# Kernel tuning notes

Hardware: AMD Instinct MI355X
Metric: run time of the kernel (lower is better)

The kernel has to match this reference:

```python
import jax, jax.numpy as jnp
import numpy as np

NUM_GRAPHS = 4096  # fixed number of segments for scatter_mean


def setup_inputs() -> dict:
    key = jax.random.key(0)
    ks = jax.random.split(key, 8)
    N, D, G = 1_000_000, 256, 256
    s = 1.0 / np.sqrt(D)
    x = jax.random.normal(ks[0], (N, D), dtype=jnp.float32)
    batch = jnp.sort(jax.random.randint(ks[1], (N,), 0, NUM_GRAPHS, dtype=jnp.int64))
    W = jax.random.normal(ks[2], (D, G), dtype=jnp.float32) * s
    b = jax.random.normal(ks[3], (G,), dtype=jnp.float32) * s
    Wg = jax.random.normal(ks[4], (D, G), dtype=jnp.float32) * s
    bg = jax.random.normal(ks[5], (G,), dtype=jnp.float32) * s
    Wf = jax.random.normal(ks[6], (G, G), dtype=jnp.float32) * (1.0 / np.sqrt(G))
    bf = jax.random.normal(ks[7], (G,), dtype=jnp.float32) * (1.0 / np.sqrt(G))
    return {"x": x, "batch": batch, "W": W, "b": b, "Wg": Wg, "bg": bg, "Wf": Wf, "bf": bf}


def reference(x, batch, W, b, Wg, bg, Wf, bf):
    # gated linear: states * softmax(gates) over feature dim (dim=1)
    states = x @ W + b                                   # [N, G]
    gates = jax.nn.softmax(x @ Wg + bg, axis=1)          # [N, G]
    gated = states * gates                               # [N, G]
    # scatter_mean over graph ids
    seg_sum = jax.ops.segment_sum(gated, batch, num_segments=NUM_GRAPHS)
    counts = jax.ops.segment_sum(jnp.ones((x.shape[0],), dtype=gated.dtype), batch,
                                 num_segments=NUM_GRAPHS)
    mean = seg_sum / jnp.maximum(counts, 1.0)[:, None]   # [NUM_GRAPHS, G]
    return mean @ Wf + bf
```

## Files before the change

kernel.cpp:

```cpp
#include <hip/hip_runtime.h>
#include <hip/hip_bf16.h>

typedef __attribute__((ext_vector_type(8))) short short8;
typedef __attribute__((ext_vector_type(4))) float f32x4;

#define D_DIM 256
#define G_DIM 256
#define NSEG 4096
#define BM 64

__device__ __forceinline__ unsigned f2bf_u(float f) {
  unsigned u = __builtin_bit_cast(unsigned, f);
  return (u + 0x7fffu + ((u >> 16) & 1u)) >> 16;
}
__device__ __forceinline__ unsigned pk_bf2(float a, float b) {
  __hip_bfloat162 h = __float22bfloat162_rn(float2{a, b});
  unsigned r;
  __builtin_memcpy(&r, &h, 4);
  return r;
}

template <int CTRL>
__device__ __forceinline__ float dpp_add(float v) {
  int x = __builtin_bit_cast(int, v);
  int y = __builtin_amdgcn_update_dpp(0, x, CTRL, 0xF, 0xF, true);
  return v + __builtin_bit_cast(float, y);
}
__device__ __forceinline__ float row16_sum(float v) {
  v = dpp_add<0xB1>(v);
  v = dpp_add<0x4E>(v);
  v = dpp_add<0x124>(v);
  v = dpp_add<0x128>(v);
  return v;
}

__global__ void wconv_kernel(const float* __restrict__ W, const float* __restrict__ Wg,
                             unsigned short* __restrict__ Wc) {
  int j = blockIdx.x;
  int k = threadIdx.x;
  float v = (j < 256) ? W[k * 256 + j] : Wg[k * 256 + (j - 256)];
  Wc[j * 256 + k] = (unsigned short)f2bf_u(v);
}

__global__ void count_kernel(const int* __restrict__ batch, int N, float* __restrict__ counts) {
  int g = blockIdx.x * blockDim.x + threadIdx.x;
  if (g >= NSEG) return;
  int lo = 0, hi = N;
  while (lo < hi) { int mid = (lo + hi) >> 1; if (batch[mid] < g) lo = mid + 1; else hi = mid; }
  int lo2 = lo, hi2 = N;
  while (lo2 < hi2) { int mid = (lo2 + hi2) >> 1; if (batch[mid] < g + 1) lo2 = mid + 1; else hi2 = mid; }
  counts[g] = (float)(lo2 - lo);
}

__global__ __launch_bounds__(512, 4) void fused_main(
    const float* __restrict__ x, const int* __restrict__ batch,
    const unsigned short* __restrict__ Wc,
    const float* __restrict__ bvec, const float* __restrict__ bgvec,
    float* __restrict__ seg, int N) {
  __shared__ __align__(16) char xs[32768];
  __shared__ __align__(16) float part[8][64];
  __shared__ __align__(16) float sinv[64];

  const int t = threadIdx.x;
  const int lane = t & 63;
  const int wid = t >> 6;
  const int lr = lane & 15;
  const int lk = lane >> 4;
  const long row0 = (long)blockIdx.x * BM;

#pragma unroll
  for (int it = 0; it < 4; ++it) {
    int rl = it * 16 + (t >> 5);
    int kb = (t & 31) * 8;
    const float4* p = (const float4*)(x + (row0 + rl) * D_DIM + kb);
    float4 v0 = p[0], v1 = p[1];
    uint4 pk;
    pk.x = pk_bf2(v0.x, v0.y);
    pk.y = pk_bf2(v0.z, v0.w);
    pk.z = pk_bf2(v1.x, v1.y);
    pk.w = pk_bf2(v1.z, v1.w);
    int byte = (rl * 512 + kb * 2) ^ ((rl & 7) << 4);
    *(uint4*)(xs + byte) = pk;
  }
  __syncthreads();

  f32x4 acc[4][4];
#pragma unroll
  for (int m = 0; m < 4; ++m)
#pragma unroll
    for (int n = 0; n < 4; ++n) acc[m][n] = (f32x4){0.f, 0.f, 0.f, 0.f};

  const int cb = wid * 32;
  __builtin_amdgcn_s_setprio(1);
#pragma unroll
  for (int kk = 0; kk < 8; ++kk) {
    const int k0 = kk * 32 + lk * 8;
    short8 a[4], bb[4];
#pragma unroll
    for (int n = 0; n < 4; ++n) {
      int col = (n < 2) ? (cb + n * 16 + lr) : (256 + cb + (n - 2) * 16 + lr);
      bb[n] = *(const short8*)(Wc + col * 256 + k0);
    }
#pragma unroll
    for (int m = 0; m < 4; ++m) {
      int row = m * 16 + lr;
      int byte = (row * 512 + k0 * 2) ^ ((row & 7) << 4);
      a[m] = *(const short8*)(xs + byte);
    }
#pragma unroll
    for (int m = 0; m < 4; ++m)
#pragma unroll
      for (int n = 0; n < 4; ++n)
        acc[m][n] = __builtin_amdgcn_mfma_f32_16x16x32_bf16(a[m], bb[n], acc[m][n], 0, 0, 0);
  }
  __builtin_amdgcn_s_setprio(0);

  int rb[4][4];
#pragma unroll
  for (int m = 0; m < 4; ++m) {
    const int4 v = *(const int4*)(batch + row0 + m * 16 + lk * 4);
    rb[m][0] = v.x; rb[m][1] = v.y; rb[m][2] = v.z; rb[m][3] = v.w;
  }
  const int g0 = batch[row0];
  const int g1 = batch[row0 + BM - 1];

  float bgv[2];
#pragma unroll
  for (int n = 0; n < 2; ++n) bgv[n] = bgvec[cb + n * 16 + lr];
#pragma unroll
  for (int m = 0; m < 4; ++m)
#pragma unroll
    for (int n = 2; n < 4; ++n)
#pragma unroll
      for (int q = 0; q < 4; ++q)
        acc[m][n][q] = __expf(acc[m][n][q] + bgv[n - 2]);

#pragma unroll
  for (int m = 0; m < 4; ++m) {
    float s[4];
#pragma unroll
    for (int q = 0; q < 4; ++q) s[q] = row16_sum(acc[m][2][q] + acc[m][3][q]);
    if (lr == 0) {
#pragma unroll
      for (int q = 0; q < 4; ++q) part[wid][m * 16 + lk * 4 + q] = s[q];
    }
  }
  __syncthreads();
  if (wid == 0) {
    float v = part[0][lane] + part[1][lane] + part[2][lane] + part[3][lane] +
              part[4][lane] + part[5][lane] + part[6][lane] + part[7][lane];
    sinv[lane] = 1.0f / v;
  }
  __syncthreads();

  float bv[2];
#pragma unroll
  for (int n = 0; n < 2; ++n) bv[n] = bvec[cb + n * 16 + lr];
  f32x4 siv[4];
#pragma unroll
  for (int m = 0; m < 4; ++m) siv[m] = *(const f32x4*)(&sinv[m * 16 + lk * 4]);
#pragma unroll
  for (int m = 0; m < 4; ++m)
#pragma unroll
    for (int n = 0; n < 2; ++n)
#pragma unroll
      for (int q = 0; q < 4; ++q)
        acc[m][n][q] = (acc[m][n][q] + bv[n]) * acc[m][n + 2][q] * siv[m][q];

  for (int g = g0; g <= g1; ++g) {
    float p[2] = {0.f, 0.f};
#pragma unroll
    for (int m = 0; m < 4; ++m)
#pragma unroll
      for (int q = 0; q < 4; ++q) {
        bool hit = (rb[m][q] == g);
#pragma unroll
        for (int n = 0; n < 2; ++n) p[n] += hit ? acc[m][n][q] : 0.f;
      }
#pragma unroll
    for (int n = 0; n < 2; ++n) {
      p[n] += __shfl_xor(p[n], 16);
      p[n] += __shfl_xor(p[n], 32);
    }
    if (lane < 16) {
#pragma unroll
      for (int n = 0; n < 2; ++n)
        atomicAdd(seg + (long)g * G_DIM + cb + n * 16 + lane, p[n]);
    }
  }
}

__global__ __launch_bounds__(256) void final_kernel(
    float* __restrict__ seg, const float* __restrict__ counts,
    const float* __restrict__ Wf, const float* __restrict__ bfv) {
  __shared__ float mlds[16][257];
  int g0 = blockIdx.x * 16;
  int t = threadIdx.x;
#pragma unroll
  for (int i = 0; i < 16; ++i) {
    float inv = 1.0f / fmaxf(counts[g0 + i], 1.0f);
    mlds[i][t] = seg[(g0 + i) * 256 + t] * inv;
  }
  __syncthreads();
  float a[16];
#pragma unroll
  for (int i = 0; i < 16; ++i) a[i] = 0.f;
  for (int k = 0; k < 256; ++k) {
    float w = Wf[k * 256 + t];
#pragma unroll
    for (int i = 0; i < 16; ++i) a[i] += mlds[i][k] * w;
  }
  float bfx = bfv[t];
#pragma unroll
  for (int i = 0; i < 16; ++i) seg[(g0 + i) * 256 + t] = a[i] + bfx;
}

extern "C" void kernel_launch(void* const* d_in, const int* in_sizes, int n_in,
                              void* d_out, int out_size, void* d_ws, size_t ws_size,
                              hipStream_t stream) {
  const float* x = (const float*)d_in[0];
  const int* batch = (const int*)d_in[1];
  const float* W = (const float*)d_in[2];
  const float* b = (const float*)d_in[3];
  const float* Wg = (const float*)d_in[4];
  const float* bg = (const float*)d_in[5];
  const float* Wf = (const float*)d_in[6];
  const float* bf = (const float*)d_in[7];
  const int N = in_sizes[0] / D_DIM;

  unsigned short* Wc = (unsigned short*)d_ws;
  float* counts = (float*)((char*)d_ws + 262144);
  float* seg = (float*)d_out;

  (void)hipMemsetAsync(d_out, 0, (size_t)out_size * sizeof(float), stream);
  hipLaunchKernelGGL(wconv_kernel, dim3(512), dim3(256), 0, stream, W, Wg, Wc);
  hipLaunchKernelGGL(count_kernel, dim3(NSEG / 256), dim3(256), 0, stream, batch, N, counts);
  hipLaunchKernelGGL(fused_main, dim3(N / BM), dim3(512), 0, stream, x, batch, Wc, b, bg, seg, N);
  hipLaunchKernelGGL(final_kernel, dim3(NSEG / 16), dim3(256), 0, stream, seg, counts, Wf, bf);
}
```

Baseline: 638.9 us.

## Use persistent blocks over contiguous tile ranges and fold output zeroing into count kernel

```diff
diff --git a/kernel.cpp b/kernel.cpp
--- a/kernel.cpp
+++ b/kernel.cpp
@@ -8,6 +8,7 @@
 #define G_DIM 256
 #define NSEG 4096
 #define BM 64
+#define NBLK 2048
 
 __device__ __forceinline__ unsigned f2bf_u(float f) {
   unsigned u = __builtin_bit_cast(unsigned, f);
@@ -42,8 +43,13 @@
   Wc[j * 256 + k] = (unsigned short)f2bf_u(v);
 }
 
-__global__ void count_kernel(const int* __restrict__ batch, int N, float* __restrict__ counts) {
+__global__ void count_kernel(const int* __restrict__ batch, int N, float* __restrict__ counts,
+                             float* __restrict__ seg) {
   int g = blockIdx.x * blockDim.x + threadIdx.x;
+  float4* s4 = (float4*)seg;
+  const float4 z = {0.f, 0.f, 0.f, 0.f};
+#pragma unroll
+  for (int i = 0; i < (NSEG * G_DIM / 4) / (NSEG); ++i) s4[i * NSEG + g] = z;
   if (g >= NSEG) return;
   int lo = 0, hi = N;
   while (lo < hi) { int mid = (lo + hi) >> 1; if (batch[mid] < g) lo = mid + 1; else hi = mid; }
@@ -66,126 +72,136 @@
   const int wid = t >> 6;
   const int lr = lane & 15;
   const int lk = lane >> 4;
-  const long row0 = (long)blockIdx.x * BM;
-
-#pragma unroll
-  for (int it = 0; it < 4; ++it) {
-    int rl = it * 16 + (t >> 5);
-    int kb = (t & 31) * 8;
-    const float4* p = (const float4*)(x + (row0 + rl) * D_DIM + kb);
-    float4 v0 = p[0], v1 = p[1];
-    uint4 pk;
-    pk.x = pk_bf2(v0.x, v0.y);
-    pk.y = pk_bf2(v0.z, v0.w);
-    pk.z = pk_bf2(v1.x, v1.y);
-    pk.w = pk_bf2(v1.z, v1.w);
-    int byte = (rl * 512 + kb * 2) ^ ((rl & 7) << 4);
-    *(uint4*)(xs + byte) = pk;
-  }
-  __syncthreads();
-
-  f32x4 acc[4][4];
-#pragma unroll
-  for (int m = 0; m < 4; ++m)
-#pragma unroll
-    for (int n = 0; n < 4; ++n) acc[m][n] = (f32x4){0.f, 0.f, 0.f, 0.f};
-
   const int cb = wid * 32;
-  __builtin_amdgcn_s_setprio(1);
-#pragma unroll
-  for (int kk = 0; kk < 8; ++kk) {
-    const int k0 = kk * 32 + lk * 8;
-    short8 a[4], bb[4];
-#pragma unroll
-    for (int n = 0; n < 4; ++n) {
-      int col = (n < 2) ? (cb + n * 16 + lr) : (256 + cb + (n - 2) * 16 + lr);
-      bb[n] = *(const short8*)(Wc + col * 256 + k0);
-    }
+  const int ntiles = N / BM;
+
+  const int q = ntiles / NBLK, r = ntiles % NBLK;
+  const int bid = blockIdx.x;
+  const int c0 = bid * q + (bid < r ? bid : r);
+  const int c1 = c0 + q + (bid < r ? 1 : 0);
+
+  float bgv[2], bv[2];
+#pragma unroll
+  for (int n = 0; n < 2; ++n) {
+    bgv[n] = bgvec[cb + n * 16 + lr];
+    bv[n] = bvec[cb + n * 16 + lr];
+  }
+
+  for (int tile = c0; tile < c1; ++tile) {
+    const long row0 = (long)tile * BM;
+
+#pragma unroll
+    for (int it = 0; it < 4; ++it) {
+      int rl = it * 16 + (t >> 5);
+      int kb = (t & 31) * 8;
+      const float4* p = (const float4*)(x + (row0 + rl) * D_DIM + kb);
+      float4 v0 = p[0], v1 = p[1];
+      uint4 pk;
+      pk.x = pk_bf2(v0.x, v0.y);
+      pk.y = pk_bf2(v0.z, v0.w);
+      pk.z = pk_bf2(v1.x, v1.y);
+      pk.w = pk_bf2(v1.z, v1.w);
+      int byte = (rl * 512 + kb * 2) ^ ((rl & 7) << 4);
+      *(uint4*)(xs + byte) = pk;
+    }
+    __syncthreads();
+
+    f32x4 acc[4][4];
+#pragma unroll
+    for (int m = 0; m < 4; ++m)
+#pragma unroll
+      for (int n = 0; n < 4; ++n) acc[m][n] = (f32x4){0.f, 0.f, 0.f, 0.f};
+
+    __builtin_amdgcn_s_setprio(1);
+#pragma unroll
+    for (int kk = 0; kk < 8; ++kk) {
+      const int k0 = kk * 32 + lk * 8;
+      short8 a[4], bb[4];
+#pragma unroll
+      for (int n = 0; n < 4; ++n) {
+        int col = (n < 2) ? (cb + n * 16 + lr) : (256 + cb + (n - 2) * 16 + lr);
+        bb[n] = *(const short8*)(Wc + col * 256 + k0);
+      }
+#pragma unroll
+      for (int m = 0; m < 4; ++m) {
+        int row = m * 16 + lr;
+        int byte = (row * 512 + k0 * 2) ^ ((row & 7) << 4);
+        a[m] = *(const short8*)(xs + byte);
+      }
+#pragma unroll
+      for (int m = 0; m < 4; ++m)
+#pragma unroll
+        for (int n = 0; n < 4; ++n)
+          acc[m][n] = __builtin_amdgcn_mfma_f32_16x16x32_bf16(a[m], bb[n], acc[m][n], 0, 0, 0);
+    }
+    __builtin_amdgcn_s_setprio(0);
+
+    int rb[4][4];
 #pragma unroll
     for (int m = 0; m < 4; ++m) {
-      int row = m * 16 + lr;
-      int byte = (row * 512 + k0 * 2) ^ ((row & 7) << 4);
-      a[m] = *(const short8*)(xs + byte);
-    }
+      const int4 v = *(const int4*)(batch + row0 + m * 16 + lk * 4);
+      rb[m][0] = v.x; rb[m][1] = v.y; rb[m][2] = v.z; rb[m][3] = v.w;
+    }
+    const int g0 = batch[row0];
+    const int g1 = batch[row0 + BM - 1];
+
 #pragma unroll
     for (int m = 0; m < 4; ++m)
 #pragma unroll
-      for (int n = 0; n < 4; ++n)
-        acc[m][n] = __builtin_amdgcn_mfma_f32_16x16x32_bf16(a[m], bb[n], acc[m][n], 0, 0, 0);
-  }
-  __builtin_amdgcn_s_setprio(0);
-
-  int rb[4][4];
-#pragma unroll
-  for (int m = 0; m < 4; ++m) {
-    const int4 v = *(const int4*)(batch + row0 + m * 16 + lk * 4);
-    rb[m][0] = v.x; rb[m][1] = v.y; rb[m][2] = v.z; rb[m][3] = v.w;
-  }
-  const int g0 = batch[row0];
-  const int g1 = batch[row0 + BM - 1];
-
-  float bgv[2];
-#pragma unroll
-  for (int n = 0; n < 2; ++n) bgv[n] = bgvec[cb + n * 16 + lr];
-#pragma unroll
-  for (int m = 0; m < 4; ++m)
-#pragma unroll
-    for (int n = 2; n < 4; ++n)
-#pragma unroll
-      for (int q = 0; q < 4; ++q)
-        acc[m][n][q] = __expf(acc[m][n][q] + bgv[n - 2]);
-
-#pragma unroll
-  for (int m = 0; m < 4; ++m) {
-    float s[4];
-#pragma unroll
-    for (int q = 0; q < 4; ++q) s[q] = row16_sum(acc[m][2][q] + acc[m][3][q]);
-    if (lr == 0) {
-#pragma unroll
-      for (int q = 0; q < 4; ++q) part[wid][m * 16 + lk * 4 + q] = s[q];
-    }
-  }
-  __syncthreads();
-  if (wid == 0) {
-    float v = part[0][lane] + part[1][lane] + part[2][lane] + part[3][lane] +
-              part[4][lane] + part[5][lane] + part[6][lane] + part[7][lane];
-    sinv[lane] = 1.0f / v;
-  }
-  __syncthreads();
-
-  float bv[2];
-#pragma unroll
-  for (int n = 0; n < 2; ++n) bv[n] = bvec[cb + n * 16 + lr];
-  f32x4 siv[4];
-#pragma unroll
-  for (int m = 0; m < 4; ++m) siv[m] = *(const f32x4*)(&sinv[m * 16 + lk * 4]);
-#pragma unroll
-  for (int m = 0; m < 4; ++m)
-#pragma unroll
-    for (int n = 0; n < 2; ++n)
-#pragma unroll
-      for (int q = 0; q < 4; ++q)
-        acc[m][n][q] = (acc[m][n][q] + bv[n]) * acc[m][n + 2][q] * siv[m][q];
-
-  for (int g = g0; g <= g1; ++g) {
-    float p[2] = {0.f, 0.f};
+      for (int n = 2; n < 4; ++n)
+#pragma unroll
+        for (int qq = 0; qq < 4; ++qq)
+          acc[m][n][qq] = __expf(acc[m][n][qq] + bgv[n - 2]);
+
+#pragma unroll
+    for (int m = 0; m < 4; ++m) {
+      float s[4];
+#pragma unroll
+      for (int qq = 0; qq < 4; ++qq) s[qq] = row16_sum(acc[m][2][qq] + acc[m][3][qq]);
+      if (lr == 0) {
+#pragma unroll
+        for (int qq = 0; qq < 4; ++qq) part[wid][m * 16 + lk * 4 + qq] = s[qq];
+      }
+    }
+    __syncthreads();
+    if (wid == 0) {
+      float v = part[0][lane] + part[1][lane] + part[2][lane] + part[3][lane] +
+                part[4][lane] + part[5][lane] + part[6][lane] + part[7][lane];
+      sinv[lane] = 1.0f / v;
+    }
+    __syncthreads();
+
+    f32x4 siv[4];
+#pragma unroll
+    for (int m = 0; m < 4; ++m) siv[m] = *(const f32x4*)(&sinv[m * 16 + lk * 4]);
 #pragma unroll
     for (int m = 0; m < 4; ++m)
 #pragma unroll
-      for (int q = 0; q < 4; ++q) {
-        bool hit = (rb[m][q] == g);
-#pragma unroll
-        for (int n = 0; n < 2; ++n) p[n] += hit ? acc[m][n][q] : 0.f;
-      }
-#pragma unroll
-    for (int n = 0; n < 2; ++n) {
-      p[n] += __shfl_xor(p[n], 16);
-      p[n] += __shfl_xor(p[n], 32);
-    }
-    if (lane < 16) {
-#pragma unroll
       for (int n = 0; n < 2; ++n)
-        atomicAdd(seg + (long)g * G_DIM + cb + n * 16 + lane, p[n]);
+#pragma unroll
+        for (int qq = 0; qq < 4; ++qq)
+          acc[m][n][qq] = (acc[m][n][qq] + bv[n]) * acc[m][n + 2][qq] * siv[m][qq];
+
+    for (int g = g0; g <= g1; ++g) {
+      float p[2] = {0.f, 0.f};
+#pragma unroll
+      for (int m = 0; m < 4; ++m)
+#pragma unroll
+        for (int qq = 0; qq < 4; ++qq) {
+          bool hit = (rb[m][qq] == g);
+#pragma unroll
+          for (int n = 0; n < 2; ++n) p[n] += hit ? acc[m][n][qq] : 0.f;
+        }
+#pragma unroll
+      for (int n = 0; n < 2; ++n) {
+        p[n] += __shfl_xor(p[n], 16);
+        p[n] += __shfl_xor(p[n], 32);
+      }
+      if (lane < 16) {
+#pragma unroll
+        for (int n = 0; n < 2; ++n)
+          atomicAdd(seg + (long)g * G_DIM + cb + n * 16 + lane, p[n]);
+      }
     }
   }
 }
@@ -232,9 +248,8 @@
   float* counts = (float*)((char*)d_ws + 262144);
   float* seg = (float*)d_out;
 
-  (void)hipMemsetAsync(d_out, 0, (size_t)out_size * sizeof(float), stream);
   hipLaunchKernelGGL(wconv_kernel, dim3(512), dim3(256), 0, stream, W, Wg, Wc);
-  hipLaunchKernelGGL(count_kernel, dim3(NSEG / 256), dim3(256), 0, stream, batch, N, counts);
-  hipLaunchKernelGGL(fused_main, dim3(N / BM), dim3(512), 0, stream, x, batch, Wc, b, bg, seg, N);
+  hipLaunchKernelGGL(count_kernel, dim3(NSEG / 256), dim3(256), 0, stream, batch, N, counts, seg);
+  hipLaunchKernelGGL(fused_main, dim3(NBLK), dim3(512), 0, stream, x, batch, Wc, b, bg, seg, N);
   hipLaunchKernelGGL(final_kernel, dim3(NSEG / 16), dim3(256), 0, stream, seg, counts, Wf, bf);
 }
```

Measured after the change: 1.151 ms. +80.1%, slower.

## Split GEMM into gate then state passes to cut registers and raise occupancy

Applied to the files above, without the earlier changes.

```diff
diff --git a/kernel.cpp b/kernel.cpp
--- a/kernel.cpp
+++ b/kernel.cpp
@@ -18,6 +18,12 @@
   unsigned r;
   __builtin_memcpy(&r, &h, 4);
   return r;
+}
+__device__ __forceinline__ float unpk_lo(unsigned u) {
+  return __builtin_bit_cast(float, u << 16);
+}
+__device__ __forceinline__ float unpk_hi(unsigned u) {
+  return __builtin_bit_cast(float, u & 0xffff0000u);
 }
 
 template <int CTRL>
@@ -42,8 +48,13 @@
   Wc[j * 256 + k] = (unsigned short)f2bf_u(v);
 }
 
-__global__ void count_kernel(const int* __restrict__ batch, int N, float* __restrict__ counts) {
+__global__ void count_kernel(const int* __restrict__ batch, int N, float* __restrict__ counts,
+                             float* __restrict__ seg) {
   int g = blockIdx.x * blockDim.x + threadIdx.x;
+  float4* s4 = (float4*)seg;
+  const float4 z = {0.f, 0.f, 0.f, 0.f};
+#pragma unroll
+  for (int i = 0; i < 64; ++i) s4[i * NSEG + g] = z;
   if (g >= NSEG) return;
   int lo = 0, hi = N;
   while (lo < hi) { int mid = (lo + hi) >> 1; if (batch[mid] < g) lo = mid + 1; else hi = mid; }
@@ -52,7 +63,7 @@
   counts[g] = (float)(lo2 - lo);
 }
 
-__global__ __launch_bounds__(512, 4) void fused_main(
+__global__ __launch_bounds__(512, 6) void fused_main(
     const float* __restrict__ x, const int* __restrict__ batch,
     const unsigned short* __restrict__ Wc,
     const float* __restrict__ bvec, const float* __restrict__ bgvec,
@@ -67,6 +78,7 @@
   const int lr = lane & 15;
   const int lk = lane >> 4;
   const long row0 = (long)blockIdx.x * BM;
+  const int cb = wid * 32;
 
 #pragma unroll
   for (int it = 0; it < 4; ++it) {
@@ -84,62 +96,58 @@
   }
   __syncthreads();
 
-  f32x4 acc[4][4];
+  f32x4 acc[4][2];
+
 #pragma unroll
   for (int m = 0; m < 4; ++m)
 #pragma unroll
-    for (int n = 0; n < 4; ++n) acc[m][n] = (f32x4){0.f, 0.f, 0.f, 0.f};
-
-  const int cb = wid * 32;
+    for (int n = 0; n < 2; ++n) acc[m][n] = (f32x4){0.f, 0.f, 0.f, 0.f};
+
   __builtin_amdgcn_s_setprio(1);
 #pragma unroll
   for (int kk = 0; kk < 8; ++kk) {
     const int k0 = kk * 32 + lk * 8;
-    short8 a[4], bb[4];
-#pragma unroll
-    for (int n = 0; n < 4; ++n) {
-      int col = (n < 2) ? (cb + n * 16 + lr) : (256 + cb + (n - 2) * 16 + lr);
-      bb[n] = *(const short8*)(Wc + col * 256 + k0);
-    }
-#pragma unroll
-    for (int m = 0; m < 4; ++m) {
-      int row = m * 16 + lr;
-      int byte = (row * 512 + k0 * 2) ^ ((row & 7) << 4);
-      a[m] = *(const short8*)(xs + byte);
-    }
+    short8 bb[2];
+#pragma unroll
+    for (int n = 0; n < 2; ++n)
+      bb[n] = *(const short8*)(Wc + (256 + cb + n * 16 + lr) * 256 + k0);
+#pragma unroll
+    for (int mb = 0; mb < 2; ++mb) {
+      short8 a[2];
+#pragma unroll
+      for (int mi = 0; mi < 2; ++mi) {
+        int row = (mb * 2 + mi) * 16 + lr;
+        int byte = (row * 512 + k0 * 2) ^ ((row & 7) << 4);
+        a[mi] = *(const short8*)(xs + byte);
+      }
+#pragma unroll
+      for (int mi = 0; mi < 2; ++mi)
+#pragma unroll
+        for (int n = 0; n < 2; ++n)
+          acc[mb * 2 + mi][n] =
+              __builtin_amdgcn_mfma_f32_16x16x32_bf16(a[mi], bb[n], acc[mb * 2 + mi][n], 0, 0, 0);
+    }
+  }
+  __builtin_amdgcn_s_setprio(0);
+
+  {
+    float bgv[2];
+#pragma unroll
+    for (int n = 0; n < 2; ++n) bgv[n] = bgvec[cb + n * 16 + lr];
 #pragma unroll
     for (int m = 0; m < 4; ++m)
 #pragma unroll
-      for (int n = 0; n < 4; ++n)
-        acc[m][n] = __builtin_amdgcn_mfma_f32_16x16x32_bf16(a[m], bb[n], acc[m][n], 0, 0, 0);
-  }
-  __builtin_amdgcn_s_setprio(0);
-
-  int rb[4][4];
-#pragma unroll
-  for (int m = 0; m < 4; ++m) {
-    const int4 v = *(const int4*)(batch + row0 + m * 16 + lk * 4);
-    rb[m][0] = v.x; rb[m][1] = v.y; rb[m][2] = v.z; rb[m][3] = v.w;
-  }
-  const int g0 = batch[row0];
-  const int g1 = batch[row0 + BM - 1];
-
-  float bgv[2];
-#pragma unroll
-  for (int n = 0; n < 2; ++n) bgv[n] = bgvec[cb + n * 16 + lr];
-#pragma unroll
-  for (int m = 0; m < 4; ++m)
-#pragma unroll
-    for (int n = 2; n < 4; ++n)
-#pragma unroll
-      for (int q = 0; q < 4; ++q)
-        acc[m][n][q] = __expf(acc[m][n][q] + bgv[n - 2]);
+      for (int n = 0; n < 2; ++n)
+#pragma unroll
+        for (int q = 0; q < 4; ++q)
+          acc[m][n][q] = __expf(acc[m][n][q] + bgv[n]);
+  }
 
 #pragma unroll
   for (int m = 0; m < 4; ++m) {
     float s[4];
 #pragma unroll
-    for (int q = 0; q < 4; ++q) s[q] = row16_sum(acc[m][2][q] + acc[m][3][q]);
+    for (int q = 0; q < 4; ++q) s[q] = row16_sum(acc[m][0][q] + acc[m][1][q]);
     if (lr == 0) {
 #pragma unroll
       for (int q = 0; q < 4; ++q) part[wid][m * 16 + lk * 4 + q] = s[q];
@@ -153,19 +161,72 @@
   }
   __syncthreads();
 
-  float bv[2];
-#pragma unroll
-  for (int n = 0; n < 2; ++n) bv[n] = bvec[cb + n * 16 + lr];
-  f32x4 siv[4];
-#pragma unroll
-  for (int m = 0; m < 4; ++m) siv[m] = *(const f32x4*)(&sinv[m * 16 + lk * 4]);
+  unsigned pkk[4][2][2];
+#pragma unroll
+  for (int m = 0; m < 4; ++m) {
+    f32x4 siv = *(const f32x4*)(&sinv[m * 16 + lk * 4]);
+#pragma unroll
+    for (int n = 0; n < 2; ++n) {
+      pkk[m][n][0] = pk_bf2(acc[m][n][0] * siv[0], acc[m][n][1] * siv[1]);
+      pkk[m][n][1] = pk_bf2(acc[m][n][2] * siv[2], acc[m][n][3] * siv[3]);
+    }
+  }
+
 #pragma unroll
   for (int m = 0; m < 4; ++m)
 #pragma unroll
+    for (int n = 0; n < 2; ++n) acc[m][n] = (f32x4){0.f, 0.f, 0.f, 0.f};
+
+  __builtin_amdgcn_s_setprio(1);
+#pragma unroll
+  for (int kk = 0; kk < 8; ++kk) {
+    const int k0 = kk * 32 + lk * 8;
+    short8 bb[2];
+#pragma unroll
     for (int n = 0; n < 2; ++n)
-#pragma unroll
-      for (int q = 0; q < 4; ++q)
-        acc[m][n][q] = (acc[m][n][q] + bv[n]) * acc[m][n + 2][q] * siv[m][q];
+      bb[n] = *(const short8*)(Wc + (cb + n * 16 + lr) * 256 + k0);
+#pragma unroll
+    for (int mb = 0; mb < 2; ++mb) {
+      short8 a[2];
+#pragma unroll
+      for (int mi = 0; mi < 2; ++mi) {
+        int row = (mb * 2 + mi) * 16 + lr;
+        int byte = (row * 512 + k0 * 2) ^ ((row & 7) << 4);
+        a[mi] = *(const short8*)(xs + byte);
+      }
+#pragma unroll
+      for (int mi = 0; mi < 2; ++mi)
+#pragma unroll
+        for (int n = 0; n < 2; ++n)
+          acc[mb * 2 + mi][n] =
+              __builtin_amdgcn_mfma_f32_16x16x32_bf16(a[mi], bb[n], acc[mb * 2 + mi][n], 0, 0, 0);
+    }
+  }
+  __builtin_amdgcn_s_setprio(0);
+
+  int rb[4][4];
+#pragma unroll
+  for (int m = 0; m < 4; ++m) {
+    const int4 v = *(const int4*)(batch + row0 + m * 16 + lk * 4);
+    rb[m][0] = v.x; rb[m][1] = v.y; rb[m][2] = v.z; rb[m][3] = v.w;
+  }
+  const int g0 = batch[row0];
+  const int g1 = batch[row0 + BM - 1];
+
+  {
+    float bv[2];
+#pragma unroll
+    for (int n = 0; n < 2; ++n) bv[n] = bvec[cb + n * 16 + lr];
+#pragma unroll
+    for (int m = 0; m < 4; ++m)
+#pragma unroll
+      for (int n = 0; n < 2; ++n) {
+        acc[m][n][0] = (acc[m][n][0] + bv[n]) * unpk_lo(pkk[m][n][0]);
+        acc[m][n][1] = (acc[m][n][1] + bv[n]) * unpk_hi(pkk[m][n][0]);
+        acc[m][n][2] = (acc[m][n][2] + bv[n]) * unpk_lo(pkk[m][n][1]);
+        acc[m][n][3] = (acc[m][n][3] + bv[n]) * unpk_hi(pkk[m][n][1]);
+      }
+  }
 
   for (int g = g0; g <= g1; ++g) {
     float p[2] = {0.f, 0.f};
@@ -232,9 +293,8 @@
   float* counts = (float*)((char*)d_ws + 262144);
   float* seg = (float*)d_out;
 
-  (void)hipMemsetAsync(d_out, 0, (size_t)out_size * sizeof(float), stream);
   hipLaunchKernelGGL(wconv_kernel, dim3(512), dim3(256), 0, stream, W, Wg, Wc);
-  hipLaunchKernelGGL(count_kernel, dim3(NSEG / 256), dim3(256), 0, stream, batch, N, counts);
+  hipLaunchKernelGGL(count_kernel, dim3(NSEG / 256), dim3(256), 0, stream, batch, N, counts, seg);
   hipLaunchKernelGGL(fused_main, dim3(N / BM), dim3(512), 0, stream, x, batch, Wc, b, bg, seg, N);
   hipLaunchKernelGGL(final_kernel, dim3(NSEG / 16), dim3(256), 0, stream, seg, counts, Wf, bf);
 }
```

Result: slower. 1.156 ms (+80.9%).

## Split row tile into two halves to overlap x loads with MFMA compute

Applied to the files above, without the earlier changes.

```diff
diff --git a/kernel.cpp b/kernel.cpp
--- a/kernel.cpp
+++ b/kernel.cpp
@@ -66,22 +66,35 @@
   const int wid = t >> 6;
   const int lr = lane & 15;
   const int lk = lane >> 4;
+  const int cb = wid * 32;
   const long row0 = (long)blockIdx.x * BM;
 
-#pragma unroll
-  for (int it = 0; it < 4; ++it) {
-    int rl = it * 16 + (t >> 5);
-    int kb = (t & 31) * 8;
-    const float4* p = (const float4*)(x + (row0 + rl) * D_DIM + kb);
+  const int srl = t >> 5;
+  const int skb = (t & 31) * 8;
+
+#pragma unroll
+  for (int it = 0; it < 2; ++it) {
+    int rl = it * 16 + srl;
+    const float4* p = (const float4*)(x + (row0 + rl) * D_DIM + skb);
     float4 v0 = p[0], v1 = p[1];
     uint4 pk;
     pk.x = pk_bf2(v0.x, v0.y);
     pk.y = pk_bf2(v0.z, v0.w);
     pk.z = pk_bf2(v1.x, v1.y);
     pk.w = pk_bf2(v1.z, v1.w);
-    int byte = (rl * 512 + kb * 2) ^ ((rl & 7) << 4);
+    int byte = (rl * 512 + skb * 2) ^ ((rl & 7) << 4);
     *(uint4*)(xs + byte) = pk;
   }
+
+  float4 LB[2][2];
+#pragma unroll
+  for (int j = 0; j < 2; ++j) {
+    int rl = (2 + j) * 16 + srl;
+    const float4* p = (const float4*)(x + (row0 + rl) * D_DIM + skb);
+    LB[j][0] = p[0];
+    LB[j][1] = p[1];
+  }
+
   __syncthreads();
 
   f32x4 acc[4][4];
@@ -90,28 +103,64 @@
 #pragma unroll
     for (int n = 0; n < 4; ++n) acc[m][n] = (f32x4){0.f, 0.f, 0.f, 0.f};
 
-  const int cb = wid * 32;
   __builtin_amdgcn_s_setprio(1);
 #pragma unroll
   for (int kk = 0; kk < 8; ++kk) {
     const int k0 = kk * 32 + lk * 8;
-    short8 a[4], bb[4];
+    short8 a[2], bb[4];
 #pragma unroll
     for (int n = 0; n < 4; ++n) {
       int col = (n < 2) ? (cb + n * 16 + lr) : (256 + cb + (n - 2) * 16 + lr);
       bb[n] = *(const short8*)(Wc + col * 256 + k0);
     }
 #pragma unroll
-    for (int m = 0; m < 4; ++m) {
+    for (int m = 0; m < 2; ++m) {
       int row = m * 16 + lr;
       int byte = (row * 512 + k0 * 2) ^ ((row & 7) << 4);
       a[m] = *(const short8*)(xs + byte);
     }
 #pragma unroll
-    for (int m = 0; m < 4; ++m)
+    for (int m = 0; m < 2; ++m)
 #pragma unroll
       for (int n = 0; n < 4; ++n)
         acc[m][n] = __builtin_amdgcn_mfma_f32_16x16x32_bf16(a[m], bb[n], acc[m][n], 0, 0, 0);
+  }
+  __builtin_amdgcn_s_setprio(0);
+
+#pragma unroll
+  for (int j = 0; j < 2; ++j) {
+    int rl = (2 + j) * 16 + srl;
+    uint4 pk;
+    pk.x = pk_bf2(LB[j][0].x, LB[j][0].y);
+    pk.y = pk_bf2(LB[j][0].z, LB[j][0].w);
+    pk.z = pk_bf2(LB[j][1].x, LB[j][1].y);
+    pk.w = pk_bf2(LB[j][1].z, LB[j][1].w);
+    int byte = (rl * 512 + skb * 2) ^ ((rl & 7) << 4);
+    *(uint4*)(xs + byte) = pk;
+  }
+  __syncthreads();
+
+  __builtin_amdgcn_s_setprio(1);
+#pragma unroll
+  for (int kk = 0; kk < 8; ++kk) {
+    const int k0 = kk * 32 + lk * 8;
+    short8 a[2], bb[4];
+#pragma unroll
+    for (int n = 0; n < 4; ++n) {
+      int col = (n < 2) ? (cb + n * 16 + lr) : (256 + cb + (n - 2) * 16 + lr);
+      bb[n] = *(const short8*)(Wc + col * 256 + k0);
+    }
+#pragma unroll
+    for (int m = 0; m < 2; ++m) {
+      int row = (m + 2) * 16 + lr;
+      int byte = (row * 512 + k0 * 2) ^ ((row & 7) << 4);
+      a[m] = *(const short8*)(xs + byte);
+    }
+#pragma unroll
+    for (int m = 0; m < 2; ++m)
+#pragma unroll
+      for (int n = 0; n < 4; ++n)
+        acc[m + 2][n] = __builtin_amdgcn_mfma_f32_16x16x32_bf16(a[m], bb[n], acc[m + 2][n], 0, 0, 0);
   }
   __builtin_amdgcn_s_setprio(0);
 
```

Result: slower. 1.060 ms (+65.9%).
